# Kernel optimization log

Measured on AMD Instinct MI355X. Metric: run time of the kernel, lower is better.

Reference implementation:

```python
import jax, jax.numpy as jnp
import numpy as np

B, N, QD = 4, 4096, 1024
HEADS, DIM_HEAD = 8, 64
HID = HEADS * DIM_HEAD
SCALE = DIM_HEAD ** -0.5


def setup_inputs() -> dict:
    key = jax.random.key(0)
    ks = jax.random.split(key, 6)
    s_in = 1.0 / np.sqrt(QD)
    s_h = 1.0 / np.sqrt(HID)
    return {
        "x": jax.random.normal(ks[0], (B, N, QD), dtype=jnp.float32),
        "Wq": jax.random.uniform(ks[1], (QD, HID), jnp.float32, -s_in, s_in),
        "Wk": jax.random.uniform(ks[2], (QD, HID), jnp.float32, -s_in, s_in),
        "Wv": jax.random.uniform(ks[3], (QD, HID), jnp.float32, -s_in, s_in),
        "Wo": jax.random.uniform(ks[4], (HID, QD), jnp.float32, -s_h, s_h),
        "bo": jax.random.uniform(ks[5], (QD,), jnp.float32, -s_h, s_h),
    }


def reference(x, Wq, Wk, Wv, Wo, bo):
    b, n, _ = x.shape
    # projections (bias-free Linears)
    q = x @ Wq  # [b, n, hid]
    k = x @ Wk
    v = x @ Wv
    # 'b n (h d) -> b h d n'
    def split_heads(t):
        return t.reshape(b, n, HEADS, DIM_HEAD).transpose(0, 2, 3, 1)  # [b,h,d,n]
    q = split_heads(q)
    k = split_heads(k)
    v = split_heads(v)
    q = jax.nn.softmax(q, axis=-2) * SCALE  # softmax over feature dim d
    k = jax.nn.softmax(k, axis=-1)          # softmax over sequence dim n
    context = jnp.einsum('bhdn,bhen->bhde', k, v)   # [b,h,d,e] small d x e
    out = jnp.einsum('bhde,bhdn->bhen', context, q)  # [b,h,e,n]
    # 'b h e n -> b n (h e)'
    out = out.transpose(0, 3, 1, 2).reshape(b, n, HID)
    return out @ Wo + bo
```

## Files before the change

kernel.cpp:

```cpp
#include <hip/hip_runtime.h>
#include <hip/hip_bf16.h>

typedef __bf16 bf16_t;
typedef bf16_t bf16x8 __attribute__((ext_vector_type(8)));
typedef float floatx4 __attribute__((ext_vector_type(4)));

#define BB 4
#define NN 4096
#define QDIM 1024
#define HEADS 8
#define DHEAD 64
#define HID 512
#define ROWS (BB*NN)
#define QKV_LD 1536

__device__ __forceinline__ float b2f(bf16_t v){ return (float)v; }
__device__ __forceinline__ bf16_t f2b(float v){ return (bf16_t)v; }

__device__ __forceinline__ bf16x8 load8(const bf16_t* p) { return *(const bf16x8*)p; }
__device__ __forceinline__ bf16x8 load8(const float* p) {
  float4 a = *(const float4*)p;
  float4 b = *(const float4*)(p + 4);
  bf16x8 r;
  r[0]=f2b(a.x); r[1]=f2b(a.y); r[2]=f2b(a.z); r[3]=f2b(a.w);
  r[4]=f2b(b.x); r[5]=f2b(b.y); r[6]=f2b(b.z); r[7]=f2b(b.w);
  return r;
}
__device__ __forceinline__ void store_out(bf16_t* p, float v){ *p = f2b(v); }
__device__ __forceinline__ void store_out(float*  p, float v){ *p = v; }

__device__ __forceinline__ void gll16(const void* g, void* l) {
  __builtin_amdgcn_global_load_lds((const __attribute__((address_space(1))) void*)g,
                                   (__attribute__((address_space(3))) void*)l,
                                   16, 0, 0);
}

static constexpr size_t OFF_QKV = 0;
static constexpr size_t OFF_WT  = 50331648;
static constexpr size_t OFF_CP  = OFF_WT + 3145728;
static constexpr size_t OFF_SPT = OFF_CP + 8388608;
static constexpr size_t OFF_W2  = OFF_SPT + 131072;
static constexpr size_t OFF_XB  = OFF_CP;

__global__ __launch_bounds__(256) void prep(
    const float* __restrict__ x,
    const float* __restrict__ Wq, const float* __restrict__ Wk,
    const float* __restrict__ Wv,
    bf16_t* __restrict__ xb, bf16_t* __restrict__ WTall) {
  __shared__ bf16_t T[64][68];
  int t = threadIdx.x;
  if (blockIdx.x < 8192) {
    size_t i = ((size_t)blockIdx.x * 256 + t) * 8;
    *(bf16x8*)&xb[i] = load8(&x[i]);
    return;
  }
  int bid = blockIdx.x - 8192;
  int z = bid >> 7;
  int rem = bid & 127;
  int r0 = (rem >> 3) * 64, c0 = (rem & 7) * 64;
  const float* in = z == 0 ? Wq : (z == 1 ? Wk : Wv);
  bf16_t* o = WTall + (size_t)z * HID * QDIM;
#pragma unroll
  for (int i = 0; i < 2; ++i) {
    int u = t + i * 256; int rr = u >> 3, c8 = (u & 7) * 8;
    bf16x8 v = load8(&in[(size_t)(r0 + rr) * HID + c0 + c8]);
#pragma unroll
    for (int j = 0; j < 8; ++j) T[c8 + j][rr] = v[j];
  }
  __syncthreads();
#pragma unroll
  for (int i = 0; i < 2; ++i) {
    int u = t + i * 256; int cr = u >> 3, r8 = (u & 7) * 8;
    bf16x8 v;
#pragma unroll
    for (int j = 0; j < 8; ++j) v[j] = T[cr][r8 + j];
    *(bf16x8*)&o[(size_t)(c0 + cr) * QDIM + r0 + r8] = v;
  }
}

template <typename OT, bool QSM>
__global__ __launch_bounds__(256, 2) void gemm128(
    const bf16_t* __restrict__ A, int lda,
    const bf16_t* __restrict__ BT, int ldb,
    OT* __restrict__ C, int ldc,
    const float* __restrict__ bias, int K) {
  __shared__ bf16_t As[128 * 32];
  __shared__ bf16_t Bs[128 * 32];
  int nwg = gridDim.x * gridDim.y;
  int wg = blockIdx.y * gridDim.x + blockIdx.x;
  int sw = (wg & 7) * (nwg >> 3) + (wg >> 3);
  int bx = sw % gridDim.x, by = sw / gridDim.x;

  int m0 = by * 128, n0 = bx * 128;
  int t = threadIdx.x;
  int w = t >> 6, lane = t & 63;
  int wm = (w >> 1) * 64, wn = (w & 1) * 64;
  int lr = lane & 15, lk = (lane >> 4) * 8;

  floatx4 acc[4][4];
#pragma unroll
  for (int mi = 0; mi < 4; ++mi)
#pragma unroll
    for (int ni = 0; ni < 4; ++ni) acc[mi][ni] = (floatx4){0.f, 0.f, 0.f, 0.f};

  for (int k0 = 0; k0 < K; k0 += 32) {
#pragma unroll
    for (int i = 0; i < 2; ++i) {
      int idx = i * 256 + t;
      int r = idx >> 2, c = (idx & 3) * 8;
      bf16_t* lbase  = (bf16_t*)As + i * 2048 + w * 512;
      bf16_t* lbaseB = (bf16_t*)Bs + i * 2048 + w * 512;
      gll16(A  + (size_t)(m0 + r) * lda + k0 + c, lbase);
      gll16(BT + (size_t)(n0 + r) * ldb + k0 + c, lbaseB);
    }
    __syncthreads();
    bf16x8 af[4], bfr[4];
#pragma unroll
    for (int mi = 0; mi < 4; ++mi) af[mi] = *(const bf16x8*)&As[(wm + mi * 16 + lr) * 32 + lk];
#pragma unroll
    for (int ni = 0; ni < 4; ++ni) bfr[ni] = *(const bf16x8*)&Bs[(wn + ni * 16 + lr) * 32 + lk];
#pragma unroll
    for (int mi = 0; mi < 4; ++mi)
#pragma unroll
      for (int ni = 0; ni < 4; ++ni)
        acc[mi][ni] = __builtin_amdgcn_mfma_f32_16x16x32_bf16(af[mi], bfr[ni], acc[mi][ni], 0, 0, 0);
    __syncthreads();
  }

  if (QSM && n0 < HID) {
#pragma unroll
    for (int mi = 0; mi < 4; ++mi)
#pragma unroll
      for (int r = 0; r < 4; ++r) {
        float m = -1e30f;
#pragma unroll
        for (int ni = 0; ni < 4; ++ni) m = fmaxf(m, acc[mi][ni][r]);
#pragma unroll
        for (int off = 1; off < 16; off <<= 1) m = fmaxf(m, __shfl_xor(m, off));
        float e0 = __expf(acc[mi][0][r] - m), e1 = __expf(acc[mi][1][r] - m);
        float e2 = __expf(acc[mi][2][r] - m), e3 = __expf(acc[mi][3][r] - m);
        float s = e0 + e1 + e2 + e3;
#pragma unroll
        for (int off = 1; off < 16; off <<= 1) s += __shfl_xor(s, off);
        float inv = 0.125f / s;
        acc[mi][0][r] = e0 * inv; acc[mi][1][r] = e1 * inv;
        acc[mi][2][r] = e2 * inv; acc[mi][3][r] = e3 * inv;
      }
  }

  int quad = (lane >> 4);
#pragma unroll
  for (int ni = 0; ni < 4; ++ni) {
    int gc = n0 + wn + ni * 16 + lr;
    float bv = (!QSM && bias) ? bias[gc] : 0.f;
#pragma unroll
    for (int mi = 0; mi < 4; ++mi)
#pragma unroll
      for (int r = 0; r < 4; ++r) {
        int gr = m0 + wm + mi * 16 + quad * 4 + r;
        store_out(&C[(size_t)gr * ldc + gc], acc[mi][ni][r] + bv);
      }
  }
}

__global__ __launch_bounds__(256, 2) void gemm_out(
    const bf16_t* __restrict__ A,
    const bf16_t* __restrict__ W2T,
    float* __restrict__ C,
    const float* __restrict__ bias) {
  __shared__ bf16_t As[256 * 32];
  __shared__ bf16_t Bs[128 * 32];
  int nwg = gridDim.x * gridDim.y;
  int wg = blockIdx.y * gridDim.x + blockIdx.x;
  int sw = (wg & 7) * (nwg >> 3) + (wg >> 3);
  int bx = sw % gridDim.x, by = sw / gridDim.x;
  int m0 = by * 256, n0 = bx * 128;
  const bf16_t* BT = W2T + (size_t)(by >> 4) * QDIM * HID;
  int t = threadIdx.x;
  int w = t >> 6, lane = t & 63;
  int lr = lane & 15, lk = (lane >> 4) * 8;

  floatx4 acc[4][8];
#pragma unroll
  for (int mi = 0; mi < 4; ++mi)
#pragma unroll
    for (int ni = 0; ni < 8; ++ni) acc[mi][ni] = (floatx4){0.f, 0.f, 0.f, 0.f};

  for (int k0 = 0; k0 < HID; k0 += 32) {
#pragma unroll
    for (int i = 0; i < 4; ++i) {
      int idx = i * 256 + t; int r = idx >> 2, c = (idx & 3) * 8;
      gll16(A + (size_t)(m0 + r) * QKV_LD + k0 + c,
            (char*)As + i * 4096 + w * 1024);
    }
#pragma unroll
    for (int i = 0; i < 2; ++i) {
      int idx = i * 256 + t; int r = idx >> 2, c = (idx & 3) * 8;
      gll16(BT + (size_t)(n0 + r) * HID + k0 + c,
            (char*)Bs + i * 4096 + w * 1024);
    }
    __syncthreads();
    bf16x8 af[4];
#pragma unroll
    for (int mi = 0; mi < 4; ++mi)
      af[mi] = *(const bf16x8*)&As[(w * 64 + mi * 16 + lr) * 32 + lk];
#pragma unroll
    for (int ni = 0; ni < 8; ++ni) {
      bf16x8 bfr = *(const bf16x8*)&Bs[(ni * 16 + lr) * 32 + lk];
#pragma unroll
      for (int mi = 0; mi < 4; ++mi)
        acc[mi][ni] = __builtin_amdgcn_mfma_f32_16x16x32_bf16(af[mi], bfr, acc[mi][ni], 0, 0, 0);
    }
    __syncthreads();
  }
  int quad = (lane >> 4);
#pragma unroll
  for (int ni = 0; ni < 8; ++ni) {
    int gc = n0 + ni * 16 + lr;
    float bv = bias[gc];
#pragma unroll
    for (int mi = 0; mi < 4; ++mi)
#pragma unroll
      for (int r = 0; r < 4; ++r) {
        int gr = m0 + w * 64 + mi * 16 + quad * 4 + r;
        C[(size_t)gr * QDIM + gc] = acc[mi][ni][r] + bv;
      }
  }
}

__global__ __launch_bounds__(256) void context_mfma(
    const bf16_t* __restrict__ qkv, float* __restrict__ cPart,
    float* __restrict__ sPart) {
  int chunk = blockIdx.x;
  int bh = blockIdx.y;
  int b = bh >> 3, h = bh & 7;
  __shared__ bf16_t ksh[64][72];
  __shared__ bf16_t vsh[64][72];
  int t = threadIdx.x;
  int w = t >> 6, lane = t & 63;
  int lr = lane & 15, lk = (lane >> 4) * 8;
  floatx4 acc[4];
  floatx4 accs = (floatx4){0.f, 0.f, 0.f, 0.f};
#pragma unroll
  for (int ni = 0; ni < 4; ++ni) acc[ni] = (floatx4){0.f, 0.f, 0.f, 0.f};
  bf16x8 ones;
#pragma unroll
  for (int j = 0; j < 8; ++j) ones[j] = f2b(1.f);

  for (int nt = 0; nt < 4; ++nt) {
    int n0 = chunk * 256 + nt * 64;
    __syncthreads();
#pragma unroll
    for (int i = 0; i < 2; ++i) {
      int u = t + i * 256; int nr = u >> 3, d8 = (u & 7) * 8;
      const bf16_t* base = qkv + (size_t)(b * NN + n0 + nr) * QKV_LD + h * 64 + d8;
      bf16x8 kv = *(const bf16x8*)(base + HID);
      bf16x8 vv = *(const bf16x8*)(base + 2 * HID);
#pragma unroll
      for (int j = 0; j < 8; ++j) {
        ksh[d8 + j][nr] = f2b(__expf(b2f(kv[j])));
        vsh[d8 + j][nr] = vv[j];
      }
    }
    __syncthreads();
#pragma unroll
    for (int s = 0; s < 2; ++s) {
      bf16x8 a = *(const bf16x8*)&ksh[w * 16 + lr][s * 32 + lk];
#pragma unroll
      for (int ni = 0; ni < 4; ++ni) {
        bf16x8 bb = *(const bf16x8*)&vsh[ni * 16 + lr][s * 32 + lk];
        acc[ni] = __builtin_amdgcn_mfma_f32_16x16x32_bf16(a, bb, acc[ni], 0, 0, 0);
      }
      accs = __builtin_amdgcn_mfma_f32_16x16x32_bf16(a, ones, accs, 0, 0, 0);
    }
  }
  float* op = cPart + (size_t)(chunk * 32 + bh) * 4096;
  int quad = lane >> 4;
#pragma unroll
  for (int ni = 0; ni < 4; ++ni)
#pragma unroll
    for (int r = 0; r < 4; ++r)
      op[(w * 16 + quad * 4 + r) * 64 + ni * 16 + lr] = acc[ni][r];
  if (lr == 0) {
#pragma unroll
    for (int r = 0; r < 4; ++r)
      sPart[(size_t)(chunk * 32 + bh) * 64 + w * 16 + quad * 4 + r] = accs[r];
  }
}

__global__ __launch_bounds__(256) void ctx2w2(
    const float* __restrict__ cPart, const float* __restrict__ sPart,
    const float* __restrict__ Wo, bf16_t* __restrict__ W2T) {
  int cchunk = blockIdx.x;
  int bh = blockIdx.y;
  int b = bh >> 3, h = bh & 7;
  __shared__ float cs[64][65];
  __shared__ float wsf[128][65];
  __shared__ float sinv[64];
  int t = threadIdx.x;
  if (t < 64) {
    float s = 0.f;
#pragma unroll 4
    for (int p = 0; p < 16; ++p) s += sPart[(size_t)(p * 32 + bh) * 64 + t];
    sinv[t] = 1.f / s;
  }
  __syncthreads();
#pragma unroll
  for (int i = 0; i < 4; ++i) {
    int f4 = t + i * 256;
    float4 s = make_float4(0.f, 0.f, 0.f, 0.f);
#pragma unroll 4
    for (int p = 0; p < 16; ++p) {
      float4 v = *(const float4*)&cPart[(size_t)(p * 32 + bh) * 4096 + f4 * 4];
      s.x += v.x; s.y += v.y; s.z += v.z; s.w += v.w;
    }
    int u = f4 * 4; int d = u >> 6, e = u & 63;
    float iv = sinv[d];
    cs[d][e] = s.x * iv; cs[d][e + 1] = s.y * iv;
    cs[d][e + 2] = s.z * iv; cs[d][e + 3] = s.w * iv;
  }
#pragma unroll
  for (int i = 0; i < 8; ++i) {
    int u = t + i * 256;
    int e = u >> 5, c4 = u & 31;
    float4 v = *(const float4*)&Wo[(size_t)(h * 64 + e) * QDIM + cchunk * 128 + c4 * 4];
    wsf[c4 * 4 + 0][e] = v.x; wsf[c4 * 4 + 1][e] = v.y;
    wsf[c4 * 4 + 2][e] = v.z; wsf[c4 * 4 + 3][e] = v.w;
  }
  __syncthreads();
  int d = t & 63;
  int cq = t >> 6;
  float rd[64];
#pragma unroll
  for (int e = 0; e < 64; ++e) rd[e] = cs[d][e];
#pragma unroll 4
  for (int ci = 0; ci < 32; ++ci) {
    int cl = cq * 32 + ci;
    float s = 0.f;
#pragma unroll
    for (int e = 0; e < 64; ++e) s += rd[e] * wsf[cl][e];
    W2T[((size_t)b * 1024 + cchunk * 128 + cl) * 512 + h * 64 + d] = f2b(s);
  }
}

extern "C" void kernel_launch(void* const* d_in, const int* in_sizes, int n_in,
                              void* d_out, int out_size, void* d_ws, size_t ws_size,
                              hipStream_t stream) {
  const float* x  = (const float*)d_in[0];
  const float* Wq = (const float*)d_in[1];
  const float* Wk = (const float*)d_in[2];
  const float* Wv = (const float*)d_in[3];
  const float* Wo = (const float*)d_in[4];
  const float* bo = (const float*)d_in[5];
  float* out = (float*)d_out;
  char* ws = (char*)d_ws;

  bf16_t* qkv   = (bf16_t*)(ws + OFF_QKV);
  bf16_t* WTall = (bf16_t*)(ws + OFF_WT);
  float*  cPart = (float*)(ws + OFF_CP);
  float*  sPart = (float*)(ws + OFF_SPT);
  bf16_t* W2T   = (bf16_t*)(ws + OFF_W2);
  bf16_t* xb    = (bf16_t*)(ws + OFF_XB);

  prep<<<8576, 256, 0, stream>>>(x, Wq, Wk, Wv, xb, WTall);

  gemm128<bf16_t, true><<<dim3(12, 128), 256, 0, stream>>>(
      xb, QDIM, WTall, QDIM, qkv, QKV_LD, nullptr, QDIM);

  context_mfma<<<dim3(16, 32), 256, 0, stream>>>(qkv, cPart, sPart);

  ctx2w2<<<dim3(8, 32), 256, 0, stream>>>(cPart, sPart, Wo, W2T);

  gemm_out<<<dim3(8, 64), 256, 0, stream>>>(qkv, W2T, out, bo);
}
```

Before: 275.5 us.

## Double GEMM K-tile to 64 with XOR-swizzled LDS, swizzle context tiles

The GEMM main loop now stages 64-wide K tiles instead of 32, halving the number of barrier pairs per K sweep and issuing two MFMA sub-steps per tile. LDS columns are XOR-swizzled by row to avoid bank conflicts on the 128-byte row stride. The context kernel's transposed K/V shared tiles also get an XOR swizzle on the 144-byte padded layout. This doubles LDS use per GEMM block, which may limit occupancy, and the swizzle in the context kernel adds address arithmetic on its scalar transposed stores.

Result: faster. 263.5 us (-4.3%).

```diff
diff --git a/kernel.cpp b/kernel.cpp
--- a/kernel.cpp
+++ b/kernel.cpp
@@ -84,8 +84,8 @@
     const bf16_t* __restrict__ BT, int ldb,
     OT* __restrict__ C, int ldc,
     const float* __restrict__ bias, int K) {
-  __shared__ bf16_t As[128 * 32];
-  __shared__ bf16_t Bs[128 * 32];
+  __shared__ bf16_t As[128 * 64];
+  __shared__ bf16_t Bs[128 * 64];
   int nwg = gridDim.x * gridDim.y;
   int wg = blockIdx.y * gridDim.x + blockIdx.x;
   int sw = (wg & 7) * (nwg >> 3) + (wg >> 3);
@@ -95,7 +95,7 @@
   int t = threadIdx.x;
   int w = t >> 6, lane = t & 63;
   int wm = (w >> 1) * 64, wn = (w & 1) * 64;
-  int lr = lane & 15, lk = (lane >> 4) * 8;
+  int lr = lane & 15;
 
   floatx4 acc[4][4];
 #pragma unroll
@@ -103,27 +103,38 @@
 #pragma unroll
     for (int ni = 0; ni < 4; ++ni) acc[mi][ni] = (floatx4){0.f, 0.f, 0.f, 0.f};
 
-  for (int k0 = 0; k0 < K; k0 += 32) {
-#pragma unroll
-    for (int i = 0; i < 2; ++i) {
+  for (int k0 = 0; k0 < K; k0 += 64) {
+#pragma unroll
+    for (int i = 0; i < 4; ++i) {
       int idx = i * 256 + t;
-      int r = idx >> 2, c = (idx & 3) * 8;
-      bf16_t* lbase  = (bf16_t*)As + i * 2048 + w * 512;
-      bf16_t* lbaseB = (bf16_t*)Bs + i * 2048 + w * 512;
-      gll16(A  + (size_t)(m0 + r) * lda + k0 + c, lbase);
-      gll16(BT + (size_t)(n0 + r) * ldb + k0 + c, lbaseB);
-    }
-    __syncthreads();
-    bf16x8 af[4], bfr[4];
-#pragma unroll
-    for (int mi = 0; mi < 4; ++mi) af[mi] = *(const bf16x8*)&As[(wm + mi * 16 + lr) * 32 + lk];
-#pragma unroll
-    for (int ni = 0; ni < 4; ++ni) bfr[ni] = *(const bf16x8*)&Bs[(wn + ni * 16 + lr) * 32 + lk];
-#pragma unroll
-    for (int mi = 0; mi < 4; ++mi)
-#pragma unroll
-      for (int ni = 0; ni < 4; ++ni)
-        acc[mi][ni] = __builtin_amdgcn_mfma_f32_16x16x32_bf16(af[mi], bfr[ni], acc[mi][ni], 0, 0, 0);
+      int r = idx >> 3, c = idx & 7;
+      int cg = c ^ (r & 7);
+      char* la = (char*)As + i * 4096 + w * 1024;
+      char* lb = (char*)Bs + i * 4096 + w * 1024;
+      gll16(A  + (size_t)(m0 + r) * lda + k0 + cg * 8, la);
+      gll16(BT + (size_t)(n0 + r) * ldb + k0 + cg * 8, lb);
+    }
+    __syncthreads();
+#pragma unroll
+    for (int s = 0; s < 2; ++s) {
+      int ci = s * 4 + (lane >> 4);
+      bf16x8 af[4], bfr[4];
+#pragma unroll
+      for (int mi = 0; mi < 4; ++mi) {
+        int row = wm + mi * 16 + lr;
+        af[mi] = *(const bf16x8*)((char*)As + row * 128 + ((ci ^ (row & 7)) * 16));
+      }
+#pragma unroll
+      for (int ni = 0; ni < 4; ++ni) {
+        int row = wn + ni * 16 + lr;
+        bfr[ni] = *(const bf16x8*)((char*)Bs + row * 128 + ((ci ^ (row & 7)) * 16));
+      }
+#pragma unroll
+      for (int mi = 0; mi < 4; ++mi)
+#pragma unroll
+        for (int ni = 0; ni < 4; ++ni)
+          acc[mi][ni] = __builtin_amdgcn_mfma_f32_16x16x32_bf16(af[mi], bfr[ni], acc[mi][ni], 0, 0, 0);
+    }
     __syncthreads();
   }
 
@@ -234,8 +245,8 @@
   int chunk = blockIdx.x;
   int bh = blockIdx.y;
   int b = bh >> 3, h = bh & 7;
-  __shared__ bf16_t ksh[64][72];
-  __shared__ bf16_t vsh[64][72];
+  __shared__ bf16_t ksh[64 * 72];
+  __shared__ bf16_t vsh[64 * 72];
   int t = threadIdx.x;
   int w = t >> 6, lane = t & 63;
   int lr = lane & 15, lk = (lane >> 4) * 8;
@@ -258,18 +269,24 @@
       bf16x8 vv = *(const bf16x8*)(base + 2 * HID);
 #pragma unroll
       for (int j = 0; j < 8; ++j) {
-        ksh[d8 + j][nr] = f2b(__expf(b2f(kv[j])));
-        vsh[d8 + j][nr] = vv[j];
+        int d = d8 + j;
+        size_t byo = ((size_t)d * 144 + nr * 2) ^ (((d >> 3) & 7) << 4);
+        *(bf16_t*)((char*)ksh + byo) = f2b(__expf(b2f(kv[j])));
+        *(bf16_t*)((char*)vsh + byo) = vv[j];
       }
     }
     __syncthreads();
 #pragma unroll
     for (int s = 0; s < 2; ++s) {
-      bf16x8 a = *(const bf16x8*)&ksh[w * 16 + lr][s * 32 + lk];
+      int arow = w * 16 + lr;
+      size_t ab = ((size_t)arow * 144 + (s * 32 + lk) * 2) ^ (((arow >> 3) & 7) << 4);
+      bf16x8 a = *(const bf16x8*)((char*)ksh + ab);
 #pragma unroll
       for (int ni = 0; ni < 4; ++ni) {
-        bf16x8 bb = *(const bf16x8*)&vsh[ni * 16 + lr][s * 32 + lk];
-        acc[ni] = __builtin_amdgcn_mfma_f32_16x16x32_bf16(a, bb, acc[ni], 0, 0, 0);
+        int brow = ni * 16 + lr;
+        size_t bb = ((size_t)brow * 144 + (s * 32 + lk) * 2) ^ (((brow >> 3) & 7) << 4);
+        bf16x8 bfr = *(const bf16x8*)((char*)vsh + bb);
+        acc[ni] = __builtin_amdgcn_mfma_f32_16x16x32_bf16(a, bfr, acc[ni], 0, 0, 0);
       }
       accs = __builtin_amdgcn_mfma_f32_16x16x32_bf16(a, ones, accs, 0, 0, 0);
     }
```
